# Kernel tuning notes

Measured on AMD Instinct MI355X. Metric: run time of the kernel, lower is better.

Reference implementation:

```python
import jax, jax.numpy as jnp
import numpy as np

B, S, H = 32, 2048, 1024

def setup_inputs() -> dict:
    key = jax.random.key(0)
    ks = jax.random.split(key, 8)
    scale = 1.0 / np.sqrt(H)
    return {
        "query": jax.random.normal(ks[0], (B, H), jnp.float32),
        "keys": jax.random.normal(ks[1], (B, S, H), jnp.float32),
        "Wa_w": jax.random.uniform(ks[2], (H, H), jnp.float32, -scale, scale),
        "Wa_b": jax.random.uniform(ks[3], (H,), jnp.float32, -scale, scale),
        "Ua_w": jax.random.uniform(ks[4], (H, H), jnp.float32, -scale, scale),
        "Ua_b": jax.random.uniform(ks[5], (H,), jnp.float32, -scale, scale),
        "Va_w": jax.random.uniform(ks[6], (1, H), jnp.float32, -scale, scale),
        "Va_b": jax.random.uniform(ks[7], (1,), jnp.float32, -scale, scale),
    }

def reference(query, keys, Wa_w, Wa_b, Ua_w, Ua_b, Va_w, Va_b):
    # q_proj: [B, 1, H]; k_proj: [B, S, H]
    q_proj = (jnp.einsum('bh,oh->bo', query, Wa_w) + Wa_b)[:, None, :]
    k_proj = jnp.einsum('bsh,oh->bso', keys, Ua_w) + Ua_b
    # scores: [B, S] via Va(tanh(...)).squeeze
    scores = jnp.einsum('bsh,h->bs', jnp.tanh(q_proj + k_proj), Va_w[0]) + Va_b[0]
    weights = jax.nn.softmax(scores, axis=1)[:, None, :]  # [B, 1, S]
    context = jnp.einsum('bqs,bsh->bqh', weights, keys)   # [B, 1, H]
    return (context, weights)
```

## Files before the change

kernel.cpp:

```cpp
#include <hip/hip_runtime.h>
#include <hip/hip_bf16.h>


#define BB 32
#define SS 2048
#define HH 1024

typedef float  f32x4  __attribute__((ext_vector_type(4)));
typedef __bf16 bf16x4 __attribute__((ext_vector_type(4)));
typedef __bf16 bf16x8 __attribute__((ext_vector_type(8)));

__device__ inline __bf16 f2bf(float f) {
  unsigned u = __builtin_bit_cast(unsigned, f);
  u = (u + 0x7FFFu + ((u >> 16) & 1u)) >> 16;
  unsigned short s = (unsigned short)u;
  return __builtin_bit_cast(__bf16, s);
}

__device__ inline float bf2f(__bf16 b) {
  unsigned short s = __builtin_bit_cast(unsigned short, b);
  unsigned u = ((unsigned)s) << 16;
  return __builtin_bit_cast(float, u);
}

__device__ inline float tanh_fast(float x) {
  x = fminf(fmaxf(x, -15.f), 15.f);
  float e = __expf(2.f * x);
  return (e - 1.f) / (e + 1.f);
}

__device__ __forceinline__ void gload16(const __bf16* g, __bf16* l) {
  __builtin_amdgcn_global_load_lds(
      (const __attribute__((address_space(1))) void*)g,
      (__attribute__((address_space(3))) void*)l, 16, 0, 0);
}

__global__ void k_convert_keys(const float* __restrict__ src, __bf16* __restrict__ dst) {
  size_t i = ((size_t)blockIdx.x * 256 + threadIdx.x) * 8;
  f32x4 a = *(const f32x4*)(src + i);
  f32x4 b = *(const f32x4*)(src + i + 4);
  bf16x8 o;
  o[0] = f2bf(a[0]); o[1] = f2bf(a[1]); o[2] = f2bf(a[2]); o[3] = f2bf(a[3]);
  o[4] = f2bf(b[0]); o[5] = f2bf(b[1]); o[6] = f2bf(b[2]); o[7] = f2bf(b[3]);
  *(bf16x8*)(dst + i) = o;
}

__global__ void k_convert_ua(const float* __restrict__ src, __bf16* __restrict__ dst) {
  size_t i = (size_t)blockIdx.x * 256 + threadIdx.x;
  f32x4 v = ((const f32x4*)src)[i];
  bf16x4 o;
  o[0] = f2bf(v[0]); o[1] = f2bf(v[1]); o[2] = f2bf(v[2]); o[3] = f2bf(v[3]);
  *(bf16x4*)(dst + i * 4) = o;
}

__global__ void k_qproj(const float* __restrict__ q, const float* __restrict__ wa,
                        const float* __restrict__ wab, const float* __restrict__ uab,
                        float* __restrict__ qpc) {
  int tid = threadIdx.x;
  int gid = blockIdx.x * 32 + (tid >> 3);
  int lane8 = tid & 7;
  int b = gid >> 10, o = gid & 1023;
  const f32x4* qv = (const f32x4*)(q + (size_t)b * HH);
  const f32x4* wv = (const f32x4*)(wa + (size_t)o * HH);
  float s = 0.f;
#pragma unroll 4
  for (int kk = lane8; kk < HH / 4; kk += 8) {
    f32x4 a = qv[kk], w = wv[kk];
    s += a[0] * w[0] + a[1] * w[1] + a[2] * w[2] + a[3] * w[3];
  }
  s += __shfl_xor(s, 1); s += __shfl_xor(s, 2); s += __shfl_xor(s, 4);
  if (lane8 == 0) qpc[(size_t)b * HH + o] = s + wab[o] + uab[o];
}

__global__ void __launch_bounds__(256) k_scores7(
    const __bf16* __restrict__ keysb, const __bf16* __restrict__ ua,
    const float* __restrict__ qpc, const float* __restrict__ vaw,
    float* __restrict__ spart) {
  __shared__ __align__(16) __bf16 Alds[2][128 * 32];
  __shared__ __align__(16) __bf16 Blds[2][128 * 32];
  __shared__ float scorebuf[128];

  int raw = blockIdx.x;
  int o = (raw >> 3) & 7;
  int m = ((raw >> 6) << 3) | (raw & 7);
  int b = m >> 4;
  long grow0 = (long)m * 128;
  int o0 = o * 128;

  int tid = threadIdx.x;
  int w = tid >> 6, lane = tid & 63;
  int wm = w >> 1, wn = w & 1;
  int ln = lane & 15, hi = lane >> 4;

  int lrow = lane >> 2;
  int g = ((lane & 3) - lrow) & 3;
  const __bf16* agA = keysb + (size_t)(grow0 + w * 16 + lrow) * HH + g * 8;
  const __bf16* agB = agA + (size_t)64 * HH;
  const __bf16* bgA = ua + (size_t)(o0 + w * 16 + lrow) * HH + g * 8;
  const __bf16* bgB = bgA + (size_t)64 * HH;
  int wofs = w * 512;

#define STAGE7(kn, bi)                                \
  do {                                                \
    int ko_ = (kn) * 32;                              \
    gload16(agA + ko_, &Alds[bi][wofs]);              \
    gload16(agB + ko_, &Alds[bi][2048 + wofs]);       \
    gload16(bgA + ko_, &Blds[bi][wofs]);              \
    gload16(bgB + ko_, &Blds[bi][2048 + wofs]);       \
  } while (0)

  int ra = (wm * 64 + ln) * 32;
  int rb = (wn * 64 + ln) * 32;
  int sa = ((hi + ln) & 3) * 8;

  f32x4 acc[4][4] = {};

  STAGE7(0, 0);
  asm volatile("s_waitcnt vmcnt(0)" ::: "memory");
  __builtin_amdgcn_s_barrier();

  for (int kt = 0; kt < 32; ++kt) {
    int cur = kt & 1;
    int kn = kt + 1 < 32 ? kt + 1 : 31;
    STAGE7(kn, cur ^ 1);
    __builtin_amdgcn_sched_barrier(0);

    const __bf16* Ab = &Alds[cur][0];
    const __bf16* Bb = &Blds[cur][0];
    bf16x8 af[4], bfr[4];
#pragma unroll
    for (int mi = 0; mi < 4; ++mi)
      af[mi] = *(const bf16x8*)(Ab + ra + mi * 512 + sa);
#pragma unroll
    for (int ni = 0; ni < 4; ++ni)
      bfr[ni] = *(const bf16x8*)(Bb + rb + ni * 512 + sa);
#pragma unroll
    for (int mi = 0; mi < 4; ++mi)
#pragma unroll
      for (int ni = 0; ni < 4; ++ni)
        acc[mi][ni] = __builtin_amdgcn_mfma_f32_16x16x32_bf16(af[mi], bfr[ni], acc[mi][ni], 0, 0, 0);

    asm volatile("s_waitcnt vmcnt(0)" ::: "memory");
    __builtin_amdgcn_s_barrier();
  }
#undef STAGE7

  float qv[4], vv[4];
#pragma unroll
  for (int ni = 0; ni < 4; ++ni) {
    int oc = o0 + wn * 64 + ni * 16 + ln;
    qv[ni] = qpc[(size_t)b * HH + oc];
    vv[ni] = vaw[oc];
  }
  float rsum[4][4];
#pragma unroll
  for (int mi = 0; mi < 4; ++mi)
#pragma unroll
    for (int j = 0; j < 4; ++j) {
      float v = 0.f;
#pragma unroll
      for (int ni = 0; ni < 4; ++ni)
        v += tanh_fast(acc[mi][ni][j] + qv[ni]) * vv[ni];
      v += __shfl_xor(v, 1); v += __shfl_xor(v, 2);
      v += __shfl_xor(v, 4); v += __shfl_xor(v, 8);
      rsum[mi][j] = v;
    }
  if (wn == 1 && ln == 0) {
#pragma unroll
    for (int mi = 0; mi < 4; ++mi)
#pragma unroll
      for (int j = 0; j < 4; ++j)
        scorebuf[wm * 64 + mi * 16 + hi * 4 + j] = rsum[mi][j];
  }
  __syncthreads();
  if (wn == 0 && ln == 0) {
#pragma unroll
    for (int mi = 0; mi < 4; ++mi)
#pragma unroll
      for (int j = 0; j < 4; ++j) {
        int rl = wm * 64 + mi * 16 + hi * 4 + j;
        spart[(size_t)o * (BB * SS) + grow0 + rl] = rsum[mi][j] + scorebuf[rl];
      }
  }
}

__global__ void __launch_bounds__(256) k_scores_fused(
    const float* __restrict__ keys, const __bf16* __restrict__ ua,
    const float* __restrict__ qpc, const float* __restrict__ vaw,
    float* __restrict__ spart) {
  __shared__ __bf16 Alds[128][40];
  __shared__ float scorebuf[128];

  int raw = blockIdx.x;
  int o = (raw >> 3) & 7;
  int m = ((raw >> 6) << 3) | (raw & 7);
  int b = m >> 4;
  long grow0 = (long)m * 128;
  int o0 = o * 128;

  int tid = threadIdx.x;
  int w = tid >> 6, lane = tid & 63;
  int wm = w >> 1, wn = w & 1;
  int ln = lane & 15, hi = lane >> 4;

  int srow = tid >> 3;
  int sk4 = tid & 7;
  const f32x4* keysv = (const f32x4*)keys;
  const bf16x8* uav = (const bf16x8*)ua;

  f32x4 acc[4][4] = {};

  for (int kt = 0; kt < 32; ++kt) {
    int k0 = kt * 32;
    bf16x8 bf[4];
#pragma unroll
    for (int ni = 0; ni < 4; ++ni) {
      int oc = o0 + wn * 64 + ni * 16 + ln;
      bf[ni] = uav[(size_t)oc * (HH / 8) + (k0 >> 3) + hi];
    }
    f32x4 st[4];
#pragma unroll
    for (int p = 0; p < 4; ++p)
      st[p] = keysv[((size_t)(grow0 + srow + 32 * p) << 8) + (size_t)(kt * 8 + sk4)];
    __syncthreads();
#pragma unroll
    for (int p = 0; p < 4; ++p) {
      bf16x4 t;
      t[0] = f2bf(st[p][0]); t[1] = f2bf(st[p][1]);
      t[2] = f2bf(st[p][2]); t[3] = f2bf(st[p][3]);
      *(bf16x4*)&Alds[srow + 32 * p][sk4 * 4] = t;
    }
    __syncthreads();
    bf16x8 af[4];
#pragma unroll
    for (int mi = 0; mi < 4; ++mi)
      af[mi] = *(const bf16x8*)&Alds[wm * 64 + mi * 16 + ln][hi * 8];
#pragma unroll
    for (int mi = 0; mi < 4; ++mi)
#pragma unroll
      for (int ni = 0; ni < 4; ++ni)
        acc[mi][ni] = __builtin_amdgcn_mfma_f32_16x16x32_bf16(af[mi], bf[ni], acc[mi][ni], 0, 0, 0);
  }

  float qv[4], vv[4];
#pragma unroll
  for (int ni = 0; ni < 4; ++ni) {
    int oc = o0 + wn * 64 + ni * 16 + ln;
    qv[ni] = qpc[(size_t)b * HH + oc];
    vv[ni] = vaw[oc];
  }
  float rsum[4][4];
#pragma unroll
  for (int mi = 0; mi < 4; ++mi)
#pragma unroll
    for (int j = 0; j < 4; ++j) {
      float v = 0.f;
#pragma unroll
      for (int ni = 0; ni < 4; ++ni)
        v += tanh_fast(acc[mi][ni][j] + qv[ni]) * vv[ni];
      v += __shfl_xor(v, 1); v += __shfl_xor(v, 2);
      v += __shfl_xor(v, 4); v += __shfl_xor(v, 8);
      rsum[mi][j] = v;
    }
  if (wn == 1 && ln == 0) {
#pragma unroll
    for (int mi = 0; mi < 4; ++mi)
#pragma unroll
      for (int j = 0; j < 4; ++j)
        scorebuf[wm * 64 + mi * 16 + hi * 4 + j] = rsum[mi][j];
  }
  __syncthreads();
  if (wn == 0 && ln == 0) {
#pragma unroll
    for (int mi = 0; mi < 4; ++mi)
#pragma unroll
      for (int j = 0; j < 4; ++j) {
        int rl = wm * 64 + mi * 16 + hi * 4 + j;
        spart[(size_t)o * (BB * SS) + grow0 + rl] = rsum[mi][j] + scorebuf[rl];
      }
  }
}

__global__ void k_softmax(const float* __restrict__ spart, float* __restrict__ wout) {
  int b = blockIdx.x, tid = threadIdx.x;
  __shared__ float red[8];
  int w = tid >> 6;
  float sc[8];
  float mx = -1e30f;
#pragma unroll
  for (int i = 0; i < 8; ++i) {
    int s = tid + i * 256;
    float v = 0.f;
#pragma unroll
    for (int ot = 0; ot < 8; ++ot) v += spart[(size_t)ot * (BB * SS) + b * SS + s];
    sc[i] = v; mx = fmaxf(mx, v);
  }
#pragma unroll
  for (int off = 1; off < 64; off <<= 1) mx = fmaxf(mx, __shfl_xor(mx, off));
  if ((tid & 63) == 0) red[w] = mx;
  __syncthreads();
  mx = fmaxf(fmaxf(red[0], red[1]), fmaxf(red[2], red[3]));
  float sum = 0.f;
#pragma unroll
  for (int i = 0; i < 8; ++i) { sc[i] = __expf(sc[i] - mx); sum += sc[i]; }
#pragma unroll
  for (int off = 1; off < 64; off <<= 1) sum += __shfl_xor(sum, off);
  if ((tid & 63) == 0) red[4 + w] = sum;
  __syncthreads();
  sum = (red[4] + red[5]) + (red[6] + red[7]);
  float inv = 1.f / sum;
#pragma unroll
  for (int i = 0; i < 8; ++i) wout[(size_t)b * SS + tid + i * 256] = sc[i] * inv;
}

__global__ void k_ctx_part_bf(const __bf16* __restrict__ keysb, const float* __restrict__ wts,
                              float* __restrict__ cpart) {
  int bc = blockIdx.x;
  int b = bc >> 4, sc = bc & 15;
  int tid = threadIdx.x;
  int s0 = sc * 128;
  f32x4 a0 = {0,0,0,0}, a1 = {0,0,0,0}, a2 = {0,0,0,0}, a3 = {0,0,0,0};
  for (int s = 0; s < 128; s += 4) {
    size_t base = (size_t)b * SS + s0 + s;
    float w0 = wts[base + 0], w1 = wts[base + 1], w2 = wts[base + 2], w3 = wts[base + 3];
    bf16x4 k0 = *(const bf16x4*)(keysb + (base + 0) * HH + tid * 4);
    bf16x4 k1 = *(const bf16x4*)(keysb + (base + 1) * HH + tid * 4);
    bf16x4 k2 = *(const bf16x4*)(keysb + (base + 2) * HH + tid * 4);
    bf16x4 k3 = *(const bf16x4*)(keysb + (base + 3) * HH + tid * 4);
#pragma unroll
    for (int j = 0; j < 4; ++j) {
      a0[j] += w0 * bf2f(k0[j]);
      a1[j] += w1 * bf2f(k1[j]);
      a2[j] += w2 * bf2f(k2[j]);
      a3[j] += w3 * bf2f(k3[j]);
    }
  }
  f32x4 a = (a0 + a1) + (a2 + a3);
  ((f32x4*)cpart)[(size_t)bc * (HH / 4) + tid] = a;
}

__global__ void k_ctx_part(const float* __restrict__ keys, const float* __restrict__ wts,
                           float* __restrict__ cpart) {
  int bc = blockIdx.x;
  int b = bc >> 4, sc = bc & 15;
  int tid = threadIdx.x;
  int s0 = sc * 128;
  const f32x4* kv = (const f32x4*)keys;
  f32x4 a0 = {0,0,0,0}, a1 = {0,0,0,0}, a2 = {0,0,0,0}, a3 = {0,0,0,0};
  for (int s = 0; s < 128; s += 4) {
    size_t base = (size_t)b * SS + s0 + s;
    a0 += wts[base + 0] * kv[(base + 0) * (HH / 4) + tid];
    a1 += wts[base + 1] * kv[(base + 1) * (HH / 4) + tid];
    a2 += wts[base + 2] * kv[(base + 2) * (HH / 4) + tid];
    a3 += wts[base + 3] * kv[(base + 3) * (HH / 4) + tid];
  }
  f32x4 a = (a0 + a1) + (a2 + a3);
  ((f32x4*)cpart)[(size_t)bc * (HH / 4) + tid] = a;
}

__global__ void k_ctx_red(const float* __restrict__ cpart, float* __restrict__ ctx) {
  int i = blockIdx.x * 256 + threadIdx.x;
  int b = i >> 10, h = i & 1023;
  float v = 0.f;
#pragma unroll
  for (int sc = 0; sc < 16; ++sc) v += cpart[((size_t)(b * 16 + sc)) * HH + h];
  ctx[i] = v;
}

extern "C" void kernel_launch(void* const* d_in, const int* in_sizes, int n_in,
                              void* d_out, int out_size, void* d_ws, size_t ws_size,
                              hipStream_t stream) {
  (void)in_sizes; (void)n_in; (void)out_size;
  const float* query = (const float*)d_in[0];
  const float* keys  = (const float*)d_in[1];
  const float* wa_w  = (const float*)d_in[2];
  const float* wa_b  = (const float*)d_in[3];
  const float* ua_w  = (const float*)d_in[4];
  const float* ua_b  = (const float*)d_in[5];
  const float* va_w  = (const float*)d_in[6];

  char* ws = (char*)d_ws;
  float* ctx_out = (float*)d_out;
  float* w_out   = ctx_out + BB * HH;

  const size_t need = (size_t)135 << 20;
  if (ws_size >= need) {
    __bf16* keys_bf = (__bf16*)ws;
    __bf16* ua_bf   = (__bf16*)(ws + ((size_t)128 << 20));
    float*  qpc     = (float*)(ws + ((size_t)130 << 20));
    float*  spart   = (float*)(ws + ((size_t)131 << 20));
    float*  cpart   = (float*)(ws + ((size_t)133 << 20));

    k_convert_keys<<<BB * SS * HH / (256 * 8), 256, 0, stream>>>(keys, keys_bf);
    k_convert_ua<<<1024, 256, 0, stream>>>(ua_w, ua_bf);
    k_qproj<<<1024, 256, 0, stream>>>(query, wa_w, wa_b, ua_b, qpc);
    k_scores7<<<4096, 256, 0, stream>>>(keys_bf, ua_bf, qpc, va_w, spart);
    k_softmax<<<BB, 256, 0, stream>>>(spart, w_out);
    k_ctx_part_bf<<<512, 256, 0, stream>>>(keys_bf, w_out, cpart);
    k_ctx_red<<<BB * HH / 256, 256, 0, stream>>>(cpart, ctx_out);
  } else {
    __bf16* ua_bf  = (__bf16*)ws;
    float*  qpc    = (float*)(ws + (2u << 20));
    float*  spart  = (float*)(ws + (2u << 20) + (128u << 10));
    float*  cpart  = (float*)(ws + (4u << 20) + (128u << 10));

    k_convert_ua<<<1024, 256, 0, stream>>>(ua_w, ua_bf);
    k_qproj<<<1024, 256, 0, stream>>>(query, wa_w, wa_b, ua_b, qpc);
    k_scores_fused<<<4096, 256, 0, stream>>>(keys, ua_bf, qpc, va_w, spart);
    k_softmax<<<BB, 256, 0, stream>>>(spart, w_out);
    k_ctx_part<<<512, 256, 0, stream>>>(keys, w_out, cpart);
    k_ctx_red<<<BB * HH / 256, 256, 0, stream>>>(cpart, ctx_out);
  }
}
```

Measured before the change: 297.7 us.

## Triple-buffer LDS in scores GEMM with two-stage-ahead prefetch and new swizzle

The scores GEMM kernel moves from double to triple buffering of its A/B tiles in shared memory. Global loads are issued two k-steps ahead, and the loop waits with vmcnt(4) instead of draining all outstanding loads each iteration. LDS fragment reads are now hoisted before the prefetch is issued. The XOR-style swizzle for the LDS layout is also changed to cut bank conflicts. This uses 50% more LDS per block, which may lower occupancy, and adds risk if the swizzle does not match between writes and reads.

```diff
diff --git a/kernel.cpp b/kernel.cpp
--- a/kernel.cpp
+++ b/kernel.cpp
@@ -72,12 +72,12 @@
   if (lane8 == 0) qpc[(size_t)b * HH + o] = s + wab[o] + uab[o];
 }
 
-__global__ void __launch_bounds__(256) k_scores7(
+__global__ void __launch_bounds__(256) k_scores8(
     const __bf16* __restrict__ keysb, const __bf16* __restrict__ ua,
     const float* __restrict__ qpc, const float* __restrict__ vaw,
     float* __restrict__ spart) {
-  __shared__ __align__(16) __bf16 Alds[2][128 * 32];
-  __shared__ __align__(16) __bf16 Blds[2][128 * 32];
+  __shared__ __align__(16) __bf16 Alds[3][128 * 32];
+  __shared__ __align__(16) __bf16 Blds[3][128 * 32];
   __shared__ float scorebuf[128];
 
   int raw = blockIdx.x;
@@ -93,57 +93,61 @@
   int ln = lane & 15, hi = lane >> 4;
 
   int lrow = lane >> 2;
-  int g = ((lane & 3) - lrow) & 3;
-  const __bf16* agA = keysb + (size_t)(grow0 + w * 16 + lrow) * HH + g * 8;
+  int sig = ((lane & 3) - ((lane >> 3) & 3)) & 3;
+  const __bf16* agA = keysb + (size_t)(grow0 + w * 16 + lrow) * HH + sig * 8;
   const __bf16* agB = agA + (size_t)64 * HH;
-  const __bf16* bgA = ua + (size_t)(o0 + w * 16 + lrow) * HH + g * 8;
+  const __bf16* bgA = ua + (size_t)(o0 + w * 16 + lrow) * HH + sig * 8;
   const __bf16* bgB = bgA + (size_t)64 * HH;
-  int wofs = w * 512;
-
-#define STAGE7(kn, bi)                                \
-  do {                                                \
-    int ko_ = (kn) * 32;                              \
-    gload16(agA + ko_, &Alds[bi][wofs]);              \
-    gload16(agB + ko_, &Alds[bi][2048 + wofs]);       \
-    gload16(bgA + ko_, &Blds[bi][wofs]);              \
-    gload16(bgB + ko_, &Blds[bi][2048 + wofs]);       \
+  int wofs = (w * 16) * 32;
+
+#define STAGE8(kn, bi)                                 \
+  do {                                                 \
+    int ko_ = (kn) * 32;                               \
+    gload16(agA + ko_, &Alds[bi][wofs]);               \
+    gload16(agB + ko_, &Alds[bi][2048 + wofs]);        \
+    gload16(bgA + ko_, &Blds[bi][wofs]);               \
+    gload16(bgB + ko_, &Blds[bi][2048 + wofs]);        \
   } while (0)
 
-  int ra = (wm * 64 + ln) * 32;
-  int rb = (wn * 64 + ln) * 32;
-  int sa = ((hi + ln) & 3) * 8;
+  int slot_a = (hi + ((ln >> 1) & 3)) & 3;
+  int ra = (wm * 64 + ln) * 32 + slot_a * 8;
+  int rb = (wn * 64 + ln) * 32 + slot_a * 8;
 
   f32x4 acc[4][4] = {};
 
-  STAGE7(0, 0);
-  asm volatile("s_waitcnt vmcnt(0)" ::: "memory");
+  STAGE8(0, 0);
+  STAGE8(1, 1);
+  asm volatile("s_waitcnt vmcnt(4)" ::: "memory");
   __builtin_amdgcn_s_barrier();
 
+  int rd = 0;
   for (int kt = 0; kt < 32; ++kt) {
-    int cur = kt & 1;
-    int kn = kt + 1 < 32 ? kt + 1 : 31;
-    STAGE7(kn, cur ^ 1);
+    const __bf16* Ab = &Alds[rd][0];
+    const __bf16* Bb = &Blds[rd][0];
+    bf16x8 af[4], bfr[4];
+#pragma unroll
+    for (int mi = 0; mi < 4; ++mi)
+      af[mi] = *(const bf16x8*)(Ab + ra + mi * 512);
+#pragma unroll
+    for (int ni = 0; ni < 4; ++ni)
+      bfr[ni] = *(const bf16x8*)(Bb + rb + ni * 512);
     __builtin_amdgcn_sched_barrier(0);
 
-    const __bf16* Ab = &Alds[cur][0];
-    const __bf16* Bb = &Blds[cur][0];
-    bf16x8 af[4], bfr[4];
-#pragma unroll
-    for (int mi = 0; mi < 4; ++mi)
-      af[mi] = *(const bf16x8*)(Ab + ra + mi * 512 + sa);
-#pragma unroll
-    for (int ni = 0; ni < 4; ++ni)
-      bfr[ni] = *(const bf16x8*)(Bb + rb + ni * 512 + sa);
+    int kn = kt + 2 < 32 ? kt + 2 : 31;
+    int wr = rd + 2; if (wr >= 3) wr -= 3;
+    STAGE8(kn, wr);
+
 #pragma unroll
     for (int mi = 0; mi < 4; ++mi)
 #pragma unroll
       for (int ni = 0; ni < 4; ++ni)
         acc[mi][ni] = __builtin_amdgcn_mfma_f32_16x16x32_bf16(af[mi], bfr[ni], acc[mi][ni], 0, 0, 0);
 
-    asm volatile("s_waitcnt vmcnt(0)" ::: "memory");
+    asm volatile("s_waitcnt vmcnt(4)" ::: "memory");
     __builtin_amdgcn_s_barrier();
-  }
-#undef STAGE7
+    rd = rd + 1; if (rd == 3) rd = 0;
+  }
+#undef STAGE8
 
   float qv[4], vv[4];
 #pragma unroll
@@ -394,7 +398,7 @@
     k_convert_keys<<<BB * SS * HH / (256 * 8), 256, 0, stream>>>(keys, keys_bf);
     k_convert_ua<<<1024, 256, 0, stream>>>(ua_w, ua_bf);
     k_qproj<<<1024, 256, 0, stream>>>(query, wa_w, wa_b, ua_b, qpc);
-    k_scores7<<<4096, 256, 0, stream>>>(keys_bf, ua_bf, qpc, va_w, spart);
+    k_scores8<<<4096, 256, 0, stream>>>(keys_bf, ua_bf, qpc, va_w, spart);
     k_softmax<<<BB, 256, 0, stream>>>(spart, w_out);
     k_ctx_part_bf<<<512, 256, 0, stream>>>(keys_bf, w_out, cpart);
     k_ctx_red<<<BB * HH / 256, 256, 0, stream>>>(cpart, ctx_out);
```

After: 286.3 us. -3.8%, faster.
